# Kernel tuning notes

Hardware: AMD Instinct MI355X
Metric: run time of the kernel (lower is better)

The kernel has to match this reference:

```python
import jax, jax.numpy as jnp
import numpy as np

PROTON = 1.00782503207
WATER = 18.0105646863
HUBER_DELTA = 0.2


def setup_inputs() -> dict:
    key = jax.random.key(0)
    k1, k2, k3, k4 = jax.random.split(key, 4)
    B, L, V, M = 512, 64, 28, 1024
    # probability distribution over vocab per position
    u = jax.random.uniform(k1, (B, L, V), dtype=jnp.float32)
    sequence_probs = u / u.sum(-1, keepdims=True)
    # observed spectrum: m/z values up to ~4000 Da, random intensities
    observed_masses = jax.random.uniform(k2, (B, M), dtype=jnp.float32) * 4000.0
    observed_intensities = jax.random.uniform(k3, (B, M), dtype=jnp.float32)
    peak_mask = jnp.ones((B, M), dtype=bool)
    # amino-acid monoisotopic masses buffer (realistic 57..186 Da range)
    aa_masses = 57.0 + jax.random.uniform(k4, (V,), dtype=jnp.float32) * 129.0
    return {
        "sequence_probs": sequence_probs,
        "observed_masses": observed_masses,
        "observed_intensities": observed_intensities,
        "peak_mask": peak_mask,
        "aa_masses": aa_masses,
    }


def _theoretical_peaks(sequence_probs, aa_masses):
    # expected residue mass per position: E[m_i] = sum_aa P(aa_i) * mass(aa)
    r = jnp.einsum("blv,v->bl", sequence_probs, aa_masses)  # (B, L)
    prefix = jnp.cumsum(r, axis=-1)                          # (B, L)
    total = prefix[:, -1:]                                   # (B, 1)
    # b ions: prefix fragments (lengths 1..L-1) + proton
    b_ions = prefix[:, :-1] + PROTON                         # (B, L-1)
    # y ions: suffix fragments + water + proton
    y_ions = total - prefix[:, :-1] + WATER + PROTON         # (B, L-1)
    return jnp.concatenate([b_ions, y_ions], axis=-1)        # (B, 2*(L-1))


def reference(sequence_probs, observed_masses, observed_intensities, peak_mask, aa_masses):
    theoretical = _theoretical_peaks(sequence_probs, aa_masses)    # (B, T)
    # pairwise |theo - obs| distance, then min over theoretical peaks
    distances = jnp.abs(theoretical[:, :, None] - observed_masses[:, None, :])  # (B, T, M)
    min_distances = distances.min(axis=1)                          # (B, M)
    huber = jnp.where(
        min_distances <= HUBER_DELTA,
        0.5 * min_distances ** 2,
        HUBER_DELTA * (min_distances - 0.5 * HUBER_DELTA),
    )
    intensity_norm = observed_intensities / jnp.clip(
        observed_intensities.sum(axis=-1, keepdims=True), 1e-8
    )
    weighted = (huber * intensity_norm * peak_mask.astype(jnp.float32)).sum(axis=-1)  # (B,)
    return weighted.mean()
```

## Files before the change

### kernel.cpp

```cpp
#include <hip/hip_runtime.h>

#define PROTON_F 1.00782503207f
#define WATER_F 18.0105646863f
#define HUBER_DELTA_F 0.2f

constexpr int B = 512;
constexpr int L = 64;
constexpr int V = 28;
constexpr int M = 1024;
constexpr int NT = 2 * (L - 1);
constexpr int NTP = 128;
constexpr int THREADS = 256;
constexpr int PROW = 29;

__global__ __launch_bounds__(THREADS)
void spectrum_loss_main(const float* __restrict__ probs,
                        const float* __restrict__ obs_mass,
                        const float* __restrict__ obs_int,
                        const int* __restrict__ mask,
                        const float* __restrict__ aa,
                        float* __restrict__ per_b)
{
    const int b = blockIdx.x;
    const int tid = threadIdx.x;
    const int lane = tid & 63;
    const int wave = tid >> 6;

    __shared__ float s_probs[L * PROW];
    __shared__ float s_prefix[L];
    __shared__ float s_T[NTP];
    __shared__ float s_red[8];

    const size_t obase = (size_t)b * M;
    const float4 om4 = ((const float4*)(obs_mass + obase))[tid];
    const float4 oi4 = ((const float4*)(obs_int + obase))[tid];
    const int4   mk4 = ((const int4*)(mask + obase))[tid];

    const float4* p4 = (const float4*)(probs + (size_t)b * (L * V));
    #pragma unroll
    for (int j = tid; j < (L * V) / 4; j += THREADS) {
        const float4 v = p4[j];
        float* dst = &s_probs[(j / 7) * PROW + (j % 7) * 4];
        dst[0] = v.x; dst[1] = v.y; dst[2] = v.z; dst[3] = v.w;
    }
    __syncthreads();

    if (tid < L) {
        float acc = 0.f;
        #pragma unroll
        for (int c = 0; c < 7; ++c) {
            const float4 a = ((const float4*)aa)[c];
            const float* pr = &s_probs[tid * PROW + c * 4];
            acc += pr[0] * a.x + pr[1] * a.y + pr[2] * a.z + pr[3] * a.w;
        }
        s_prefix[tid] = acc;
    }
    __syncthreads();

    if (tid == 0) {
        float acc = 0.f;
        for (int l = 0; l < L; ++l) { acc += s_prefix[l]; s_prefix[l] = acc; }
    }
    __syncthreads();

    if (tid < NTP) {
        float tv = 1e30f;
        if (tid < L - 1)     tv = s_prefix[tid] + PROTON_F;
        else if (tid < NT)   tv = s_prefix[L - 1] - s_prefix[tid - (L - 1)]
                                  + WATER_F + PROTON_F;
        s_T[tid] = tv;
    }
    __syncthreads();

    float mind0 = 1e30f, mind1 = 1e30f, mind2 = 1e30f, mind3 = 1e30f;
    #pragma unroll 8
    for (int t = 0; t < NTP; t += 4) {
        const float4 tv = *(const float4*)&s_T[t];
        mind0 = fminf(mind0, fabsf(tv.x - om4.x));
        mind1 = fminf(mind1, fabsf(tv.x - om4.y));
        mind2 = fminf(mind2, fabsf(tv.x - om4.z));
        mind3 = fminf(mind3, fabsf(tv.x - om4.w));
        mind0 = fminf(mind0, fabsf(tv.y - om4.x));
        mind1 = fminf(mind1, fabsf(tv.y - om4.y));
        mind2 = fminf(mind2, fabsf(tv.y - om4.z));
        mind3 = fminf(mind3, fabsf(tv.y - om4.w));
        mind0 = fminf(mind0, fabsf(tv.z - om4.x));
        mind1 = fminf(mind1, fabsf(tv.z - om4.y));
        mind2 = fminf(mind2, fabsf(tv.z - om4.z));
        mind3 = fminf(mind3, fabsf(tv.z - om4.w));
        mind0 = fminf(mind0, fabsf(tv.w - om4.x));
        mind1 = fminf(mind1, fabsf(tv.w - om4.y));
        mind2 = fminf(mind2, fabsf(tv.w - om4.z));
        mind3 = fminf(mind3, fabsf(tv.w - om4.w));
    }

    float wsum = 0.f, isum = 0.f;
    {
        float d, h;
        d = mind0; h = (d <= HUBER_DELTA_F) ? 0.5f * d * d
                                            : HUBER_DELTA_F * (d - 0.5f * HUBER_DELTA_F);
        wsum += h * oi4.x * (float)mk4.x;  isum += oi4.x;
        d = mind1; h = (d <= HUBER_DELTA_F) ? 0.5f * d * d
                                            : HUBER_DELTA_F * (d - 0.5f * HUBER_DELTA_F);
        wsum += h * oi4.y * (float)mk4.y;  isum += oi4.y;
        d = mind2; h = (d <= HUBER_DELTA_F) ? 0.5f * d * d
                                            : HUBER_DELTA_F * (d - 0.5f * HUBER_DELTA_F);
        wsum += h * oi4.z * (float)mk4.z;  isum += oi4.z;
        d = mind3; h = (d <= HUBER_DELTA_F) ? 0.5f * d * d
                                            : HUBER_DELTA_F * (d - 0.5f * HUBER_DELTA_F);
        wsum += h * oi4.w * (float)mk4.w;  isum += oi4.w;
    }

    #pragma unroll
    for (int off = 32; off > 0; off >>= 1) {
        wsum += __shfl_down(wsum, off, 64);
        isum += __shfl_down(isum, off, 64);
    }
    if (lane == 0) { s_red[wave] = wsum; s_red[4 + wave] = isum; }
    __syncthreads();

    if (tid == 0) {
        const float w = s_red[0] + s_red[1] + s_red[2] + s_red[3];
        const float i = s_red[4] + s_red[5] + s_red[6] + s_red[7];
        per_b[b] = w / fmaxf(i, 1e-8f);
    }
}

__global__ __launch_bounds__(64)
void final_reduce_wave(const float* __restrict__ per_b, float* __restrict__ out)
{
    const int lane = threadIdx.x;
    const float4 a = ((const float4*)per_b)[lane * 2];
    const float4 c = ((const float4*)per_b)[lane * 2 + 1];
    float v = (a.x + a.y) + (a.z + a.w) + (c.x + c.y) + (c.z + c.w);
    #pragma unroll
    for (int off = 32; off > 0; off >>= 1)
        v += __shfl_down(v, off, 64);
    if (lane == 0) out[0] = v * (1.0f / (float)B);
}

extern "C" void kernel_launch(void* const* d_in, const int* in_sizes, int n_in,
                              void* d_out, int out_size, void* d_ws, size_t ws_size,
                              hipStream_t stream)
{
    const float* probs = (const float*)d_in[0];
    const float* omass = (const float*)d_in[1];
    const float* oint  = (const float*)d_in[2];
    const int*   pmask = (const int*)d_in[3];
    const float* aa    = (const float*)d_in[4];
    float* out  = (float*)d_out;
    float* perb = (float*)d_ws;

    spectrum_loss_main<<<B, THREADS, 0, stream>>>(probs, omass, oint, pmask, aa, perb);
    final_reduce_wave<<<1, 64, 0, stream>>>(perb, out);
}
```

Baseline: 11.73 us.

## Replace brute-force nearest-peak search with binary search over sorted b/y ions

Because the prefix sums of positive residue masses are monotonic, b ions come out sorted ascending and y ions sorted descending. The change stores y ions in reversed order, so both arrays are sorted, and finds each observed mass's nearest theoretical peak with a 6-step binary search per array instead of scanning all 128 candidates. It also replaces the serial single-thread prefix sum with a wave-level shuffle scan, which removes two block barriers. The binary search brings data-dependent LDS gathers that can cause bank conflicts, and its correctness relies on residue masses being positive so the arrays stay sorted.

```diff
diff --git a/kernel.cpp b/kernel.cpp
--- a/kernel.cpp
+++ b/kernel.cpp
@@ -8,10 +8,9 @@
 constexpr int L = 64;
 constexpr int V = 28;
 constexpr int M = 1024;
-constexpr int NT = 2 * (L - 1);
-constexpr int NTP = 128;
 constexpr int THREADS = 256;
 constexpr int PROW = 29;
+
 
 __global__ __launch_bounds__(THREADS)
 void spectrum_loss_main(const float* __restrict__ probs,
@@ -27,8 +26,8 @@
     const int wave = tid >> 6;
 
     __shared__ float s_probs[L * PROW];
-    __shared__ float s_prefix[L];
-    __shared__ float s_T[NTP];
+    __shared__ float s_bA[64];
+    __shared__ float s_yA[64];
     __shared__ float s_red[8];
 
     const size_t obase = (size_t)b * M;
@@ -45,53 +44,56 @@
     }
     __syncthreads();
 
-    if (tid < L) {
-        float acc = 0.f;
+    if (wave == 0) {
+        float r = 0.f;
         #pragma unroll
         for (int c = 0; c < 7; ++c) {
             const float4 a = ((const float4*)aa)[c];
-            const float* pr = &s_probs[tid * PROW + c * 4];
-            acc += pr[0] * a.x + pr[1] * a.y + pr[2] * a.z + pr[3] * a.w;
+            const float* pr = &s_probs[lane * PROW + c * 4];
+            r += pr[0] * a.x + pr[1] * a.y + pr[2] * a.z + pr[3] * a.w;
         }
-        s_prefix[tid] = acc;
+        float pref = r;
+        #pragma unroll
+        for (int off = 1; off < 64; off <<= 1) {
+            const float t = __shfl_up(pref, off, 64);
+            if (lane >= off) pref += t;
+        }
+        const float total = __shfl(pref, 63, 64);
+        s_bA[lane] = (lane < 63) ? pref + PROTON_F : 1e30f;
+        if (lane < 63) s_yA[62 - lane] = total - pref + WATER_F + PROTON_F;
+        else           s_yA[63] = 1e30f;
     }
     __syncthreads();
 
-    if (tid == 0) {
-        float acc = 0.f;
-        for (int l = 0; l < L; ++l) { acc += s_prefix[l]; s_prefix[l] = acc; }
+    const float omv0 = om4.x, omv1 = om4.y, omv2 = om4.z, omv3 = om4.w;
+    int ib0 = 0, ib1 = 0, ib2 = 0, ib3 = 0;
+    int iy0 = 0, iy1 = 0, iy2 = 0, iy3 = 0;
+    #pragma unroll
+    for (int k = 32; k >= 1; k >>= 1) {
+        ib0 += (s_bA[ib0 + k - 1] < omv0) ? k : 0;
+        ib1 += (s_bA[ib1 + k - 1] < omv1) ? k : 0;
+        ib2 += (s_bA[ib2 + k - 1] < omv2) ? k : 0;
+        ib3 += (s_bA[ib3 + k - 1] < omv3) ? k : 0;
+        iy0 += (s_yA[iy0 + k - 1] < omv0) ? k : 0;
+        iy1 += (s_yA[iy1 + k - 1] < omv1) ? k : 0;
+        iy2 += (s_yA[iy2 + k - 1] < omv2) ? k : 0;
+        iy3 += (s_yA[iy3 + k - 1] < omv3) ? k : 0;
     }
-    __syncthreads();
-
-    if (tid < NTP) {
-        float tv = 1e30f;
-        if (tid < L - 1)     tv = s_prefix[tid] + PROTON_F;
-        else if (tid < NT)   tv = s_prefix[L - 1] - s_prefix[tid - (L - 1)]
-                                  + WATER_F + PROTON_F;
-        s_T[tid] = tv;
-    }
-    __syncthreads();
-
-    float mind0 = 1e30f, mind1 = 1e30f, mind2 = 1e30f, mind3 = 1e30f;
-    #pragma unroll 8
-    for (int t = 0; t < NTP; t += 4) {
-        const float4 tv = *(const float4*)&s_T[t];
-        mind0 = fminf(mind0, fabsf(tv.x - om4.x));
-        mind1 = fminf(mind1, fabsf(tv.x - om4.y));
-        mind2 = fminf(mind2, fabsf(tv.x - om4.z));
-        mind3 = fminf(mind3, fabsf(tv.x - om4.w));
-        mind0 = fminf(mind0, fabsf(tv.y - om4.x));
-        mind1 = fminf(mind1, fabsf(tv.y - om4.y));
-        mind2 = fminf(mind2, fabsf(tv.y - om4.z));
-        mind3 = fminf(mind3, fabsf(tv.y - om4.w));
-        mind0 = fminf(mind0, fabsf(tv.z - om4.x));
-        mind1 = fminf(mind1, fabsf(tv.z - om4.y));
-        mind2 = fminf(mind2, fabsf(tv.z - om4.z));
-        mind3 = fminf(mind3, fabsf(tv.z - om4.w));
-        mind0 = fminf(mind0, fabsf(tv.w - om4.x));
-        mind1 = fminf(mind1, fabsf(tv.w - om4.y));
-        mind2 = fminf(mind2, fabsf(tv.w - om4.z));
-        mind3 = fminf(mind3, fabsf(tv.w - om4.w));
+    float mind0, mind1, mind2, mind3;
+    {
+        float db, dy;
+        db = fminf(fabsf(s_bA[ib0] - omv0), fabsf(s_bA[ib0 - (ib0 > 0)] - omv0));
+        dy = fminf(fabsf(s_yA[iy0] - omv0), fabsf(s_yA[iy0 - (iy0 > 0)] - omv0));
+        mind0 = fminf(db, dy);
+        db = fminf(fabsf(s_bA[ib1] - omv1), fabsf(s_bA[ib1 - (ib1 > 0)] - omv1));
+        dy = fminf(fabsf(s_yA[iy1] - omv1), fabsf(s_yA[iy1 - (iy1 > 0)] - omv1));
+        mind1 = fminf(db, dy);
+        db = fminf(fabsf(s_bA[ib2] - omv2), fabsf(s_bA[ib2 - (ib2 > 0)] - omv2));
+        dy = fminf(fabsf(s_yA[iy2] - omv2), fabsf(s_yA[iy2 - (iy2 > 0)] - omv2));
+        mind2 = fminf(db, dy);
+        db = fminf(fabsf(s_bA[ib3] - omv3), fabsf(s_bA[ib3 - (ib3 > 0)] - omv3));
+        dy = fminf(fabsf(s_yA[iy3] - omv3), fabsf(s_yA[iy3 - (iy3 > 0)] - omv3));
+        mind3 = fminf(db, dy);
     }
 
     float wsum = 0.f, isum = 0.f;
```

Result: faster. 11.20 us (-4.6%).
